# Performance work log

Hardware: AMD Instinct MI355X
Metric: run time of the kernel (lower is better)

Reference implementation:

```python
import jax, jax.numpy as jnp
import numpy as np

N_NODES, N_EDGES, N_EVAL = 100000, 1600000, 200000
IN_C, HID_C, OUT_C = 128, 256, 128


def setup_inputs() -> dict:
    key = jax.random.key(0)
    ks = jax.random.split(key, 10)
    x = jax.random.normal(ks[0], (N_NODES, IN_C), dtype=jnp.float32)
    edge_index = jax.random.randint(ks[1], (2, N_EDGES), 0, N_NODES)
    pos_edge_index = jax.random.randint(ks[2], (2, N_EVAL), 0, N_NODES)
    neg_edge_index = jax.random.randint(ks[3], (2, N_EVAL), 0, N_NODES)

    def glorot(k, fi, fo):
        return jax.random.normal(k, (fi, fo), dtype=jnp.float32) * np.float32(1.0 / np.sqrt(fi))

    W1 = glorot(ks[4], IN_C, HID_C); b1 = jnp.zeros((HID_C,), jnp.float32)
    W2 = glorot(ks[5], HID_C, HID_C); b2 = jnp.zeros((HID_C,), jnp.float32)
    W3 = glorot(ks[6], HID_C, OUT_C); b3 = jnp.zeros((OUT_C,), jnp.float32)
    return dict(x=x, edge_index=edge_index, pos_edge_index=pos_edge_index,
                neg_edge_index=neg_edge_index, W1=W1, b1=b1, W2=W2, b2=b2, W3=W3, b3=b3)


def gcn_layer(x, W, b, src, dst, deg_inv_sqrt):
    # GCNConv: D^{-1/2} (A + I) D^{-1/2} X W + b, degrees include self-loops.
    h = x @ W                                            # [N, F_out]
    norm = deg_inv_sqrt[src] * deg_inv_sqrt[dst]         # [E]
    msg = h[src] * norm[:, None]                          # [E, F_out] gathered messages
    agg = jax.ops.segment_sum(msg, dst, num_segments=x.shape[0])
    agg = agg + h * (deg_inv_sqrt * deg_inv_sqrt)[:, None]  # self-loop contribution
    return agg + b


def reference(x, edge_index, pos_edge_index, neg_edge_index, W1, b1, W2, b2, W3, b3):
    n = x.shape[0]
    src, dst = edge_index[0], edge_index[1]
    # in-degree with self-loops
    deg = jax.ops.segment_sum(jnp.ones_like(dst, dtype=x.dtype), dst, num_segments=n) + 1.0
    dis = jax.lax.rsqrt(deg)
    # encode (index=0); dropout is identity in eval mode
    h = jax.nn.relu(gcn_layer(x, W1, b1, src, dst, dis))
    h = jax.nn.relu(gcn_layer(h, W2, b2, src, dst, dis))
    z = gcn_layer(h, W3, b3, src, dst, dis)
    # decode: per-edge dot product over pos + neg eval edges
    ei = jnp.concatenate([pos_edge_index, neg_edge_index], axis=1)
    logits = jnp.sum(z[ei[0]] * z[ei[1]], axis=-1)
    return logits
```

## Files before the change

kernel.cpp:

```cpp
#include <hip/hip_runtime.h>
#include <cstdint>
#include <cstddef>

#define N_NODES 100000
#define N_EDGES 1600000
#define N_EVAL  200000

typedef __attribute__((ext_vector_type(8))) short bf16x8;
typedef __attribute__((ext_vector_type(4))) float f32x4;
typedef __attribute__((ext_vector_type(2))) float f32x2;
typedef __attribute__((ext_vector_type(4))) unsigned int u32x4;
typedef __attribute__((ext_vector_type(2))) unsigned int u32x2;
typedef __attribute__((ext_vector_type(8))) unsigned short u16x8;

__device__ __forceinline__ unsigned short f2bf_rne(float f) {
    unsigned int u = __float_as_uint(f);
    unsigned int r = (u + 0x7FFFu + ((u >> 16) & 1u)) >> 16;
    return (unsigned short)r;
}
__device__ __forceinline__ float bf2f(unsigned short h) {
    return __uint_as_float(((unsigned int)h) << 16);
}
__device__ __forceinline__ unsigned int pack_bf(float v) {
    unsigned short h = f2bf_rne(v);
    unsigned short l = f2bf_rne(v - bf2f(h));
    return ((unsigned int)h << 16) | (unsigned int)l;
}


__global__ void count_deg_kernel(const int* __restrict__ dst, int* __restrict__ deg, int E) {
    int i = blockIdx.x * blockDim.x + threadIdx.x;
    if (i < E) atomicAdd(&deg[dst[i]], 1);
}

__global__ void dis_kernel(const int* __restrict__ deg, float* __restrict__ dis, int N) {
    int i = blockIdx.x * blockDim.x + threadIdx.x;
    if (i < N) dis[i] = rsqrtf((float)deg[i] + 1.0f);
}

__global__ __launch_bounds__(1024) void scan_kernel(const int* __restrict__ deg,
                                                    int* __restrict__ offsets, int N, int E) {
    __shared__ int sums[1024];
    int t = threadIdx.x;
    int C = (N + 1023) >> 10;
    int lo = t * C;
    int hi = min(lo + C, N);
    int s = 0;
    for (int i = lo; i < hi; ++i) s += deg[i];
    sums[t] = s;
    __syncthreads();
    for (int d = 1; d < 1024; d <<= 1) {
        int add = (t >= d) ? sums[t - d] : 0;
        __syncthreads();
        sums[t] += add;
        __syncthreads();
    }
    int run = sums[t] - s;
    for (int i = lo; i < hi; ++i) { offsets[i] = run; run += deg[i]; }
    if (hi >= N) offsets[N] = E;
}

__global__ void fill_csr_kernel(const int* __restrict__ src, const int* __restrict__ dst,
                                const float* __restrict__ dis, int* __restrict__ cursor,
                                int2* __restrict__ csr, int E) {
    int e = blockIdx.x * blockDim.x + threadIdx.x;
    if (e < E) {
        int s = src[e], d = dst[e];
        int p = atomicAdd(&cursor[d], 1);
        csr[p] = make_int2(s, __float_as_int(dis[s] * dis[d]));
    }
}


__global__ void wsplit_kernel(const float* __restrict__ W, unsigned short* __restrict__ Wt_hi,
                              unsigned short* __restrict__ Wt_lo, int K, int N) {
    int idx = blockIdx.x * blockDim.x + threadIdx.x;
    if (idx >= K * N) return;
    int k = idx / N, n = idx - k * N;
    float v = W[idx];
    unsigned short h = f2bf_rne(v);
    Wt_hi[(size_t)n * K + k] = h;
    Wt_lo[(size_t)n * K + k] = f2bf_rne(v - bf2f(h));
}


#define KP 40

template <bool BIAS, bool RELU, bool PACKOUT>
__global__ __launch_bounds__(256, 2) void gemm_bf16split_kernel(
    const unsigned int* __restrict__ A,
    const unsigned short* __restrict__ Wt_hi,
    const unsigned short* __restrict__ Wt_lo,
    void* __restrict__ Cout, int M, int N, int K,
    const float* __restrict__ bias)
{
    __shared__ unsigned short As_hi[128][KP];
    __shared__ unsigned short As_lo[128][KP];
    __shared__ unsigned short Bs_hi[128][KP];
    __shared__ unsigned short Bs_lo[128][KP];

    const int tid = threadIdx.x;
    const int m0 = blockIdx.x * 128;
    const int n0 = blockIdx.y * 128;
    const int lane = tid & 63;
    const int wave = tid >> 6;
    const int wm0 = (wave >> 1) * 64;
    const int wn0 = (wave & 1) * 64;
    const int fr = lane & 15;
    const int fk = (lane >> 4) * 8;

    f32x4 acc[4][4];
#pragma unroll
    for (int i = 0; i < 4; ++i)
#pragma unroll
        for (int j = 0; j < 4; ++j) acc[i][j] = (f32x4){0.f, 0.f, 0.f, 0.f};

    const int srow = tid >> 1;
    const int sc0 = (tid & 1) * 16;
    const int agrow = m0 + srow;
    const unsigned int* Ap = A + (size_t)agrow * K + sc0;
    const unsigned short* Bh = Wt_hi + (size_t)(n0 + srow) * K + sc0;
    const unsigned short* Bl = Wt_lo + (size_t)(n0 + srow) * K + sc0;

    for (int k0 = 0; k0 < K; k0 += 32) {
        unsigned int ua[16];
        if (agrow < M) {
            *(u32x4*)(ua)      = *(const u32x4*)(Ap + k0);
            *(u32x4*)(ua + 4)  = *(const u32x4*)(Ap + k0 + 4);
            *(u32x4*)(ua + 8)  = *(const u32x4*)(Ap + k0 + 8);
            *(u32x4*)(ua + 12) = *(const u32x4*)(Ap + k0 + 12);
        } else {
#pragma unroll
            for (int i = 0; i < 16; ++i) ua[i] = 0u;
        }
        unsigned short h[16], l[16];
#pragma unroll
        for (int i = 0; i < 16; ++i) {
            h[i] = (unsigned short)(ua[i] >> 16);
            l[i] = (unsigned short)(ua[i] & 0xFFFFu);
        }
        *(u16x8*)&As_hi[srow][sc0]     = *(const u16x8*)(h);
        *(u16x8*)&As_hi[srow][sc0 + 8] = *(const u16x8*)(h + 8);
        *(u16x8*)&As_lo[srow][sc0]     = *(const u16x8*)(l);
        *(u16x8*)&As_lo[srow][sc0 + 8] = *(const u16x8*)(l + 8);
        *(u16x8*)&Bs_hi[srow][sc0]     = *(const u16x8*)(Bh + k0);
        *(u16x8*)&Bs_hi[srow][sc0 + 8] = *(const u16x8*)(Bh + k0 + 8);
        *(u16x8*)&Bs_lo[srow][sc0]     = *(const u16x8*)(Bl + k0);
        *(u16x8*)&Bs_lo[srow][sc0 + 8] = *(const u16x8*)(Bl + k0 + 8);
        __syncthreads();

        bf16x8 af_h[4], af_l[4], bf_h[4], bf_l[4];
#pragma unroll
        for (int i = 0; i < 4; ++i) {
            af_h[i] = *(const bf16x8*)&As_hi[wm0 + i * 16 + fr][fk];
            af_l[i] = *(const bf16x8*)&As_lo[wm0 + i * 16 + fr][fk];
            bf_h[i] = *(const bf16x8*)&Bs_hi[wn0 + i * 16 + fr][fk];
            bf_l[i] = *(const bf16x8*)&Bs_lo[wn0 + i * 16 + fr][fk];
        }
#pragma unroll
        for (int i = 0; i < 4; ++i)
#pragma unroll
            for (int j = 0; j < 4; ++j) {
                acc[i][j] = __builtin_amdgcn_mfma_f32_16x16x32_bf16(af_h[i], bf_h[j], acc[i][j], 0, 0, 0);
                acc[i][j] = __builtin_amdgcn_mfma_f32_16x16x32_bf16(af_l[i], bf_h[j], acc[i][j], 0, 0, 0);
                acc[i][j] = __builtin_amdgcn_mfma_f32_16x16x32_bf16(af_h[i], bf_l[j], acc[i][j], 0, 0, 0);
            }
        __syncthreads();
    }

    float* Cf = (float*)Cout;
    unsigned int* Cp = (unsigned int*)Cout;
#pragma unroll
    for (int j = 0; j < 4; ++j) {
        const int col = n0 + wn0 + j * 16 + fr;
        const float bb = BIAS ? bias[col] : 0.f;
#pragma unroll
        for (int i = 0; i < 4; ++i) {
            const int rbase = m0 + wm0 + i * 16 + (lane >> 4) * 4;
#pragma unroll
            for (int r = 0; r < 4; ++r) {
                const int row = rbase + r;
                if (row < M) {
                    float v = acc[i][j][r] + bb;
                    if (RELU) v = fmaxf(v, 0.f);
                    if (PACKOUT) {
                        __builtin_nontemporal_store(pack_bf(v), &Cp[(size_t)row * N + col]);
                    } else {
                        __builtin_nontemporal_store(v, &Cf[(size_t)row * N + col]);
                    }
                }
            }
        }
    }
}


template <int VEC>
__device__ __forceinline__ void vload(float (&r)[VEC], const float* __restrict__ p) {
    if constexpr (VEC == 4) {
        float4 v = *(const float4*)p;
        r[0] = v.x; r[1] = v.y; r[2] = v.z; r[3] = v.w;
    } else {
        float2 v = *(const float2*)p;
        r[0] = v.x; r[1] = v.y;
    }
}

template <int F, bool BIAS, bool RELU, bool PACKOUT>
__global__ __launch_bounds__(256) void aggregate_vec_kernel(
    const float* __restrict__ H,
    const int* __restrict__ offsets,
    const int2* __restrict__ csr,
    const float* __restrict__ dis,
    const float* __restrict__ bias,
    void* __restrict__ OUT, int N)
{
    constexpr int VEC = F / 64;
    const int node = blockIdx.x * 4 + (threadIdx.x >> 6);
    if (node >= N) return;
    const int lane = threadIdx.x & 63;
    const int col = lane * VEC;

    const float d = dis[node];
    float acc[VEC];
    {
        float v[VEC];
        vload<VEC>(v, H + (size_t)node * F + col);
        const float dd = d * d;
#pragma unroll
        for (int q = 0; q < VEC; ++q) acc[q] = v[q] * dd;
    }

    const int e0 = offsets[node], e1 = offsets[node + 1];
    int e = e0;
    for (; e + 4 <= e1; e += 4) {
        int2 c0 = csr[e], c1 = csr[e + 1], c2 = csr[e + 2], c3 = csr[e + 3];
        float v0[VEC], v1[VEC], v2[VEC], v3[VEC];
        vload<VEC>(v0, H + (size_t)c0.x * F + col);
        vload<VEC>(v1, H + (size_t)c1.x * F + col);
        vload<VEC>(v2, H + (size_t)c2.x * F + col);
        vload<VEC>(v3, H + (size_t)c3.x * F + col);
        const float w0 = __int_as_float(c0.y), w1 = __int_as_float(c1.y);
        const float w2 = __int_as_float(c2.y), w3 = __int_as_float(c3.y);
#pragma unroll
        for (int q = 0; q < VEC; ++q) acc[q] = fmaf(w0, v0[q], acc[q]);
#pragma unroll
        for (int q = 0; q < VEC; ++q) acc[q] = fmaf(w1, v1[q], acc[q]);
#pragma unroll
        for (int q = 0; q < VEC; ++q) acc[q] = fmaf(w2, v2[q], acc[q]);
#pragma unroll
        for (int q = 0; q < VEC; ++q) acc[q] = fmaf(w3, v3[q], acc[q]);
    }
    for (; e < e1; ++e) {
        int2 c0 = csr[e];
        float v0[VEC];
        vload<VEC>(v0, H + (size_t)c0.x * F + col);
        const float w0 = __int_as_float(c0.y);
#pragma unroll
        for (int q = 0; q < VEC; ++q) acc[q] = fmaf(w0, v0[q], acc[q]);
    }

    if (BIAS) {
        float b[VEC];
        vload<VEC>(b, bias + col);
#pragma unroll
        for (int q = 0; q < VEC; ++q) acc[q] += b[q];
    }
    if (RELU) {
#pragma unroll
        for (int q = 0; q < VEC; ++q) acc[q] = fmaxf(acc[q], 0.f);
    }

    if constexpr (PACKOUT) {
        unsigned int* op = (unsigned int*)OUT + (size_t)node * F + col;
        if constexpr (VEC == 4) {
            u32x4 u = {pack_bf(acc[0]), pack_bf(acc[1]), pack_bf(acc[2]), pack_bf(acc[3])};
            __builtin_nontemporal_store(u, (u32x4*)op);
        } else {
            u32x2 u = {pack_bf(acc[0]), pack_bf(acc[1])};
            __builtin_nontemporal_store(u, (u32x2*)op);
        }
    } else {
        float* op = (float*)OUT + (size_t)node * F + col;
        if constexpr (VEC == 4) {
            f32x4 v = {acc[0], acc[1], acc[2], acc[3]};
            __builtin_nontemporal_store(v, (f32x4*)op);
        } else {
            f32x2 v = {acc[0], acc[1]};
            __builtin_nontemporal_store(v, (f32x2*)op);
        }
    }
}


__global__ __launch_bounds__(256) void decode_kernel(const float* __restrict__ z,
                                                     const int* __restrict__ pos,
                                                     const int* __restrict__ neg,
                                                     float* __restrict__ out)
{
    const int wave = threadIdx.x >> 6;
    const int lane = threadIdx.x & 63;
    const int ebase = (blockIdx.x * 4 + wave) * 4;
    if (ebase >= 2 * N_EVAL) return;
    int ia[4], ib[4];
#pragma unroll
    for (int q = 0; q < 4; ++q) {
        const int e = ebase + q;
        if (e < N_EVAL) { ia[q] = pos[e];          ib[q] = pos[N_EVAL + e]; }
        else            { ia[q] = neg[e - N_EVAL]; ib[q] = neg[e]; }
    }
    float2 za[4], zb[4];
#pragma unroll
    for (int q = 0; q < 4; ++q) {
        za[q] = *(const float2*)(z + (size_t)ia[q] * 128 + lane * 2);
        zb[q] = *(const float2*)(z + (size_t)ib[q] * 128 + lane * 2);
    }
    float v[4];
#pragma unroll
    for (int q = 0; q < 4; ++q) v[q] = za[q].x * zb[q].x + za[q].y * zb[q].y;
#pragma unroll
    for (int d = 32; d > 0; d >>= 1) {
#pragma unroll
        for (int q = 0; q < 4; ++q) v[q] += __shfl_xor(v[q], d);
    }
    if (lane == 0) {
#pragma unroll
        for (int q = 0; q < 4; ++q) out[ebase + q] = v[q];
    }
}


extern "C" void kernel_launch(void* const* d_in, const int* in_sizes, int n_in,
                              void* d_out, int out_size, void* d_ws, size_t ws_size,
                              hipStream_t stream)
{
    const float* x  = (const float*)d_in[0];
    const int*   ei = (const int*)d_in[1];
    const int*  pos = (const int*)d_in[2];
    const int*  neg = (const int*)d_in[3];
    const float* W1 = (const float*)d_in[4];
    const float* b1 = (const float*)d_in[5];
    const float* W2 = (const float*)d_in[6];
    const float* b2 = (const float*)d_in[7];
    const float* W3 = (const float*)d_in[8];
    const float* b3 = (const float*)d_in[9];
    float* out = (float*)d_out;

    const int N = N_NODES, E = N_EDGES;

    char* p = (char*)d_ws;
    auto alloc = [&](size_t bytes) {
        char* r = p;
        p += (bytes + 255) & ~(size_t)255;
        return r;
    };
    int*   deg     = (int*)  alloc((size_t)N * 4);
    int*   offsets = (int*)  alloc((size_t)(N + 1) * 4);
    int*   cursor  = (int*)  alloc((size_t)N * 4);
    float* dis     = (float*)alloc((size_t)N * 4);
    int2*  csr     = (int2*) alloc((size_t)E * 8);
    char*  bufA    = (char*) alloc((size_t)N * 256 * 4);
    char*  bufB    = (char*) alloc((size_t)N * 256 * 4);
    unsigned short* W1h = (unsigned short*)alloc((size_t)256 * 128 * 2);
    unsigned short* W1l = (unsigned short*)alloc((size_t)256 * 128 * 2);
    unsigned short* W2h = (unsigned short*)alloc((size_t)256 * 256 * 2);
    unsigned short* W2l = (unsigned short*)alloc((size_t)256 * 256 * 2);
    unsigned short* W3h = (unsigned short*)alloc((size_t)128 * 256 * 2);
    unsigned short* W3l = (unsigned short*)alloc((size_t)128 * 256 * 2);

    const int* src = ei;
    const int* dst = ei + E;

    wsplit_kernel<<<(128 * 256 + 255) / 256, 256, 0, stream>>>(W1, W1h, W1l, 128, 256);
    wsplit_kernel<<<(256 * 256 + 255) / 256, 256, 0, stream>>>(W2, W2h, W2l, 256, 256);
    wsplit_kernel<<<(256 * 128 + 255) / 256, 256, 0, stream>>>(W3, W3h, W3l, 256, 128);

    hipMemsetAsync(deg, 0, (size_t)N * 4, stream);
    count_deg_kernel<<<(E + 255) / 256, 256, 0, stream>>>(dst, deg, E);
    dis_kernel<<<(N + 255) / 256, 256, 0, stream>>>(deg, dis, N);
    scan_kernel<<<1, 1024, 0, stream>>>(deg, offsets, N, E);
    hipMemcpyAsync(cursor, offsets, (size_t)N * 4, hipMemcpyDeviceToDevice, stream);
    fill_csr_kernel<<<(E + 255) / 256, 256, 0, stream>>>(src, dst, dis, cursor, csr, E);

    const int agg_grid = (N + 3) / 4;
    const int mblocks = (N + 127) / 128;

    aggregate_vec_kernel<128, false, false, true><<<agg_grid, 256, 0, stream>>>(
        x, offsets, csr, dis, nullptr, bufA, N);
    gemm_bf16split_kernel<true, true, true><<<dim3(mblocks, 2), 256, 0, stream>>>(
        (const unsigned int*)bufA, W1h, W1l, bufB, N, 256, 128, b1);

    gemm_bf16split_kernel<false, false, false><<<dim3(mblocks, 2), 256, 0, stream>>>(
        (const unsigned int*)bufB, W2h, W2l, bufA, N, 256, 256, nullptr);
    aggregate_vec_kernel<256, true, true, true><<<agg_grid, 256, 0, stream>>>(
        (const float*)bufA, offsets, csr, dis, b2, bufB, N);

    gemm_bf16split_kernel<false, false, false><<<dim3(mblocks, 1), 256, 0, stream>>>(
        (const unsigned int*)bufB, W3h, W3l, bufA, N, 128, 256, nullptr);
    aggregate_vec_kernel<128, true, false, false><<<agg_grid, 256, 0, stream>>>(
        (const float*)bufA, offsets, csr, dis, b3, bufB, N);

    decode_kernel<<<(2 * N_EVAL + 15) / 16, 256, 0, stream>>>(
        (const float*)bufB, pos, neg, out);
}
```

Measured before the change: 1.040 ms.

## Fuse dis and cursor init into scan, prefetch GEMM tiles, use regular stores

Folds the dis computation and the cursor copy into the single-block scan kernel, which removes one kernel launch and one device-to-device memcpy. The GEMM main loop now prefetches the next K-tile of A and B into registers before the barrier, so global loads overlap the MFMA work at the cost of extra registers. Nontemporal stores in the GEMM and aggregate epilogues become ordinary stores, so the intermediate buffers can stay in cache for the next kernel. The single-block scan now does more serial work per thread.

```diff
diff --git a/kernel.cpp b/kernel.cpp
--- a/kernel.cpp
+++ b/kernel.cpp
@@ -33,13 +33,11 @@
     if (i < E) atomicAdd(&deg[dst[i]], 1);
 }
 
-__global__ void dis_kernel(const int* __restrict__ deg, float* __restrict__ dis, int N) {
-    int i = blockIdx.x * blockDim.x + threadIdx.x;
-    if (i < N) dis[i] = rsqrtf((float)deg[i] + 1.0f);
-}
-
 __global__ __launch_bounds__(1024) void scan_kernel(const int* __restrict__ deg,
-                                                    int* __restrict__ offsets, int N, int E) {
+                                                    int* __restrict__ offsets,
+                                                    int* __restrict__ cursor,
+                                                    float* __restrict__ dis,
+                                                    int N, int E) {
     __shared__ int sums[1024];
     int t = threadIdx.x;
     int C = (N + 1023) >> 10;
@@ -56,7 +54,12 @@
         __syncthreads();
     }
     int run = sums[t] - s;
-    for (int i = lo; i < hi; ++i) { offsets[i] = run; run += deg[i]; }
+    for (int i = lo; i < hi; ++i) {
+        offsets[i] = run;
+        cursor[i] = run;
+        dis[i] = rsqrtf((float)deg[i] + 1.0f);
+        run += deg[i];
+    }
     if (hi >= N) offsets[N] = E;
 }
 
@@ -122,17 +125,29 @@
     const unsigned short* Bh = Wt_hi + (size_t)(n0 + srow) * K + sc0;
     const unsigned short* Bl = Wt_lo + (size_t)(n0 + srow) * K + sc0;
 
-    for (int k0 = 0; k0 < K; k0 += 32) {
-        unsigned int ua[16];
-        if (agrow < M) {
-            *(u32x4*)(ua)      = *(const u32x4*)(Ap + k0);
-            *(u32x4*)(ua + 4)  = *(const u32x4*)(Ap + k0 + 4);
-            *(u32x4*)(ua + 8)  = *(const u32x4*)(Ap + k0 + 8);
-            *(u32x4*)(ua + 12) = *(const u32x4*)(Ap + k0 + 12);
-        } else {
-#pragma unroll
-            for (int i = 0; i < 16; ++i) ua[i] = 0u;
-        }
+    unsigned int ua[16];
+    u16x8 rbh[2], rbl[2];
+
+#define LOADG(K0)                                                     \
+    do {                                                              \
+        if (agrow < M) {                                              \
+            *(u32x4*)(ua)      = *(const u32x4*)(Ap + (K0));          \
+            *(u32x4*)(ua + 4)  = *(const u32x4*)(Ap + (K0) + 4);      \
+            *(u32x4*)(ua + 8)  = *(const u32x4*)(Ap + (K0) + 8);      \
+            *(u32x4*)(ua + 12) = *(const u32x4*)(Ap + (K0) + 12);     \
+        } else {                                                      \
+            _Pragma("unroll") for (int z = 0; z < 16; ++z) ua[z] = 0u;\
+        }                                                             \
+        rbh[0] = *(const u16x8*)(Bh + (K0));                          \
+        rbh[1] = *(const u16x8*)(Bh + (K0) + 8);                      \
+        rbl[0] = *(const u16x8*)(Bl + (K0));                          \
+        rbl[1] = *(const u16x8*)(Bl + (K0) + 8);                      \
+    } while (0)
+
+    LOADG(0);
+    const int niter = K >> 5;
+
+    for (int it = 0; it < niter; ++it) {
         unsigned short h[16], l[16];
 #pragma unroll
         for (int i = 0; i < 16; ++i) {
@@ -143,10 +158,11 @@
         *(u16x8*)&As_hi[srow][sc0 + 8] = *(const u16x8*)(h + 8);
         *(u16x8*)&As_lo[srow][sc0]     = *(const u16x8*)(l);
         *(u16x8*)&As_lo[srow][sc0 + 8] = *(const u16x8*)(l + 8);
-        *(u16x8*)&Bs_hi[srow][sc0]     = *(const u16x8*)(Bh + k0);
-        *(u16x8*)&Bs_hi[srow][sc0 + 8] = *(const u16x8*)(Bh + k0 + 8);
-        *(u16x8*)&Bs_lo[srow][sc0]     = *(const u16x8*)(Bl + k0);
-        *(u16x8*)&Bs_lo[srow][sc0 + 8] = *(const u16x8*)(Bl + k0 + 8);
+        *(u16x8*)&Bs_hi[srow][sc0]     = rbh[0];
+        *(u16x8*)&Bs_hi[srow][sc0 + 8] = rbh[1];
+        *(u16x8*)&Bs_lo[srow][sc0]     = rbl[0];
+        *(u16x8*)&Bs_lo[srow][sc0 + 8] = rbl[1];
+        if (it + 1 < niter) LOADG((it + 1) << 5);
         __syncthreads();
 
         bf16x8 af_h[4], af_l[4], bf_h[4], bf_l[4];
@@ -167,6 +183,7 @@
             }
         __syncthreads();
     }
+#undef LOADG
 
     float* Cf = (float*)Cout;
     unsigned int* Cp = (unsigned int*)Cout;
@@ -183,11 +200,8 @@
                 if (row < M) {
                     float v = acc[i][j][r] + bb;
                     if (RELU) v = fmaxf(v, 0.f);
-                    if (PACKOUT) {
-                        __builtin_nontemporal_store(pack_bf(v), &Cp[(size_t)row * N + col]);
-                    } else {
-                        __builtin_nontemporal_store(v, &Cf[(size_t)row * N + col]);
-                    }
+                    if (PACKOUT) Cp[(size_t)row * N + col] = pack_bf(v);
+                    else         Cf[(size_t)row * N + col] = v;
                 }
             }
         }
@@ -274,20 +288,16 @@
     if constexpr (PACKOUT) {
         unsigned int* op = (unsigned int*)OUT + (size_t)node * F + col;
         if constexpr (VEC == 4) {
-            u32x4 u = {pack_bf(acc[0]), pack_bf(acc[1]), pack_bf(acc[2]), pack_bf(acc[3])};
-            __builtin_nontemporal_store(u, (u32x4*)op);
+            *(u32x4*)op = (u32x4){pack_bf(acc[0]), pack_bf(acc[1]), pack_bf(acc[2]), pack_bf(acc[3])};
         } else {
-            u32x2 u = {pack_bf(acc[0]), pack_bf(acc[1])};
-            __builtin_nontemporal_store(u, (u32x2*)op);
+            *(u32x2*)op = (u32x2){pack_bf(acc[0]), pack_bf(acc[1])};
         }
     } else {
         float* op = (float*)OUT + (size_t)node * F + col;
         if constexpr (VEC == 4) {
-            f32x4 v = {acc[0], acc[1], acc[2], acc[3]};
-            __builtin_nontemporal_store(v, (f32x4*)op);
+            *(float4*)op = make_float4(acc[0], acc[1], acc[2], acc[3]);
         } else {
-            f32x2 v = {acc[0], acc[1]};
-            __builtin_nontemporal_store(v, (f32x2*)op);
+            *(float2*)op = make_float2(acc[0], acc[1]);
         }
     }
 }
@@ -377,9 +387,7 @@
 
     hipMemsetAsync(deg, 0, (size_t)N * 4, stream);
     count_deg_kernel<<<(E + 255) / 256, 256, 0, stream>>>(dst, deg, E);
-    dis_kernel<<<(N + 255) / 256, 256, 0, stream>>>(deg, dis, N);
-    scan_kernel<<<1, 1024, 0, stream>>>(deg, offsets, N, E);
-    hipMemcpyAsync(cursor, offsets, (size_t)N * 4, hipMemcpyDeviceToDevice, stream);
+    scan_kernel<<<1, 1024, 0, stream>>>(deg, offsets, cursor, dis, N, E);
     fill_csr_kernel<<<(E + 255) / 256, 256, 0, stream>>>(src, dst, dis, cursor, csr, E);
 
     const int agg_grid = (N + 3) / 4;
```

New measurement: 1.129 ms. 8.6% more time.
